# Kernel optimization log

Measured on AMD Instinct MI355X. Metric: run time of the kernel, lower is better.

The kernel has to match this reference:

```python
import jax, jax.numpy as jnp
import numpy as np
from jax import lax

VOCAB = 50257; IN_DIM = 1024; MEM = 1024
ATT_UNITS = 256; HOPS = 16
H1 = 1024; H2 = 512; H3 = 256; CLASSES = 5
N = 512  # maxlen == number of tree nodes (pad() is a no-op, penalty mask is zero)


def _build_tree(n):
    # Binary heap tree relabeled to DFS post-order ranks, so children always
    # have smaller rank than their parent and H accumulates in the same order
    # as the original recursive torch code.
    order = []
    def post(j):
        for c in (2 * j + 1, 2 * j + 2):
            if c < n:
                post(c)
        order.append(j)
    post(0)
    rank = {j: r for r, j in enumerate(order)}
    child_idx = np.zeros((n, 2), np.int32)
    mask = np.zeros((n, 2), np.float32)
    for j in range(n):
        r = rank[j]
        for k, c in enumerate((2 * j + 1, 2 * j + 2)):
            if c < n:
                child_idx[r, k] = rank[c]
                mask[r, k] = 1.0
    return jnp.asarray(child_idx), jnp.asarray(mask)


def setup_inputs() -> dict:
    key = jax.random.key(0)
    ks = jax.random.split(key, 24)
    def w(k, shape, s=0.05):
        return jax.random.normal(k, shape, jnp.float32) * s
    child_idx, child_mask = _build_tree(N)
    return {
        "linputs": jax.random.randint(ks[0], (N,), 0, VOCAB, jnp.int32),
        "rinputs": jax.random.randint(ks[1], (N,), 0, VOCAB, jnp.int32),
        "child_idx": child_idx,
        "child_mask": child_mask,
        "emb": w(ks[2], (VOCAB, IN_DIM)),
        "w_ioux": w(ks[3], (3 * MEM, IN_DIM)), "b_ioux": w(ks[4], (3 * MEM,)),
        "w_iouh": w(ks[5], (3 * MEM, MEM)), "b_iouh": w(ks[6], (3 * MEM,)),
        "w_fx": w(ks[7], (MEM, IN_DIM)), "b_fx": w(ks[8], (MEM,)),
        "w_fh": w(ks[9], (MEM, MEM)), "b_fh": w(ks[10], (MEM,)),
        "ws1": w(ks[11], (ATT_UNITS, MEM)),
        "ws2": w(ks[12], (HOPS, ATT_UNITS)),
        "wf": w(ks[13], (1, MEM, H1)),
        "w_lat": w(ks[14], (1, HOPS)), "b_lat": w(ks[15], (1,)),
        "w_fc": w(ks[16], (H2, 3 * H1)), "b_fc": w(ks[17], (H2,)),
        "w_out": w(ks[18], (H3, H2)), "b_out": w(ks[19], (H3,)),
        "w_out1": w(ks[20], (CLASSES, H3)), "b_out1": w(ks[21], (CLASSES,)),
    }


def _tree_lstm(x, child_idx, child_mask, w_ioux, b_ioux, w_iouh, b_iouh,
               w_fx, b_fx, w_fh, b_fh):
    # x: [N, in_dim]; nodes in post-order (children before parent).
    # Leaf case of the original (single all-zero child) is reproduced exactly
    # by masked (zero) child rows: child_h_sum = 0 and sum(f * child_c) = 0.
    n = x.shape[0]
    mem = w_fh.shape[0]
    x_iou = x @ w_ioux.T + b_ioux  # [N, 3M], precomputed input projections
    x_f = x @ w_fx.T + b_fx        # [N, M]

    def step(carry, xs):
        C, Hs = carry
        i, ci, m, xiou, xf = xs
        ch = Hs[ci] * m[:, None]   # [2, M] masked child hidden states
        cc = C[ci] * m[:, None]    # [2, M] masked child cell states
        iou = xiou + ch.sum(0) @ w_iouh.T + b_iouh
        ig, og, ug = jnp.split(iou, 3)
        ig = jax.nn.sigmoid(ig); og = jax.nn.sigmoid(og); ug = jnp.tanh(ug)
        f = jax.nn.sigmoid(ch @ w_fh.T + b_fh + xf)  # [2, M] forget per child
        c = ig * ug + (f * cc).sum(0)
        h = og * jnp.tanh(c)
        return (C.at[i].set(c), Hs.at[i].set(h)), None

    z = jnp.zeros((n, mem), x.dtype)
    (C, Hs), _ = lax.scan(step, (z, z),
                          (jnp.arange(n), child_idx, child_mask, x_iou, x_f))
    return Hs  # H stacked in DFS post-order; root hidden is Hs[-1]


def _attend(H, ws1, ws2):
    # H: [N, M]; N == maxlen so the penalty term of the original is all-zero.
    hbar = jnp.tanh(H @ ws1.T)                           # [N, att_units]
    alphas = jax.nn.softmax((hbar @ ws2.T).T, axis=-1)   # [hops, N]
    return alphas @ H, alphas[None]                      # [hops, M], [1, hops, N]


def reference(linputs, rinputs, child_idx, child_mask, emb,
              w_ioux, b_ioux, w_iouh, b_iouh, w_fx, b_fx, w_fh, b_fh,
              ws1, ws2, wf, w_lat, b_lat, w_fc, b_fc, w_out, b_out,
              w_out1, b_out1):
    tl = lambda tok: _tree_lstm(emb[tok], child_idx, child_mask,
                                w_ioux, b_ioux, w_iouh, b_iouh,
                                w_fx, b_fx, w_fh, b_fh)
    Hl = tl(linputs)
    Hr = tl(rinputs)
    Ml, attl = _attend(Hl, ws1, ws2)
    Mr, attr = _attend(Hr, ws1, ws2)
    lstate = jax.nn.relu(Ml @ wf[0])   # [hops, H1]
    rstate = jax.nn.relu(Mr @ wf[0])
    # lat_att applied on transposed matrix == left-multiply by its weight row
    lvec = w_lat @ lstate + b_lat      # [1, H1]
    rvec = w_lat @ rstate + b_lat
    fr = jnp.concatenate([jnp.abs(lvec - rvec), lvec * rvec,
                          0.5 * (lvec + rvec)], axis=1)  # [1, 3*H1]
    fc = jax.nn.leaky_relu(fr @ w_fc.T + b_fc, 0.01)
    fc2 = jax.nn.sigmoid(fc @ w_out.T + b_out)
    out = jax.nn.log_softmax(fc2 @ w_out1.T + b_out1, axis=-1)  # [1, classes]
    return out, attl, attr
```

## Files before the change

kernel.cpp:

```cpp
#include <hip/hip_runtime.h>
#include <math.h>

#define NN 512
#define MEMD 1024

typedef __attribute__((ext_vector_type(8))) short short8;
typedef __attribute__((ext_vector_type(4))) float float4v;

struct Sched {
  int child0[NN]; int child1[NN];
  float m0[NN]; float m1[NN];
  int chrow[2 * NN];
  int order[NN];
  int lvl_off[12];
};

constexpr void post_order_rec(int j, int n, int (&ord)[NN], int& cnt) {
  if (2 * j + 1 < n) post_order_rec(2 * j + 1, n, ord, cnt);
  if (2 * j + 2 < n) post_order_rec(2 * j + 2, n, ord, cnt);
  ord[cnt++] = j;
}

constexpr Sched make_sched() {
  Sched s{};
  int ord[NN] = {}; int cnt = 0;
  post_order_rec(0, NN, ord, cnt);
  int rank[NN] = {};
  for (int r = 0; r < NN; ++r) rank[ord[r]] = r;
  for (int j = 0; j < NN; ++j) {
    int r = rank[j];
    int c0 = 2 * j + 1, c1 = 2 * j + 2;
    s.child0[r] = (c0 < NN) ? rank[c0] : 0;
    s.m0[r] = (c0 < NN) ? 1.0f : 0.0f;
    s.child1[r] = (c1 < NN) ? rank[c1] : 0;
    s.m1[r] = (c1 < NN) ? 1.0f : 0.0f;
  }
  int h[NN] = {};
  for (int r = 0; r < NN; ++r) {
    int hh = 0;
    if (s.m0[r] > 0.0f) { int t = h[s.child0[r]] + 1; if (t > hh) hh = t; }
    if (s.m1[r] > 0.0f) { int t = h[s.child1[r]] + 1; if (t > hh) hh = t; }
    h[r] = hh;
  }
  int counts[12] = {};
  for (int r = 0; r < NN; ++r) counts[h[r]]++;
  s.lvl_off[0] = 0;
  for (int l = 0; l < 11; ++l) s.lvl_off[l + 1] = s.lvl_off[l] + counts[l];
  int pos[12] = {};
  for (int l = 0; l < 12; ++l) pos[l] = s.lvl_off[l];
  for (int r = 0; r < NN; ++r) s.order[pos[h[r]]++] = r;
  for (int slot = 0; slot < NN; ++slot) {
    int r = s.order[slot];
    s.chrow[2 * slot + 0] = (s.m0[r] > 0.f) ? s.child0[r] : -1;
    s.chrow[2 * slot + 1] = (s.m1[r] > 0.f) ? s.child1[r] : -1;
  }
  return s;
}

static constexpr Sched g_sched = make_sched();
__constant__ Sched c_sched = g_sched;

__device__ __forceinline__ float sigm(float x) { return 1.0f / (1.0f + expf(-x)); }

__device__ __forceinline__ unsigned short f2bf(float f) {
  union { float f; unsigned int u; } v; v.f = f;
  unsigned int r = v.u + 0x7fffu + ((v.u >> 16) & 1u);
  return (unsigned short)(r >> 16);
}

__device__ __forceinline__ void glds16(const unsigned short* g, unsigned short* l) {
  __builtin_amdgcn_global_load_lds(
      (const __attribute__((address_space(1))) void*)g,
      (__attribute__((address_space(3))) void*)l, 16, 0, 0);
}

__global__ __launch_bounds__(256) void k_cast_w(
    const float* __restrict__ w_ioux, const float* __restrict__ w_fx,
    const float* __restrict__ w_iouh, const float* __restrict__ w_fh,
    unsigned short* __restrict__ Wx, unsigned short* __restrict__ Wh)
{
  const int b = (int)blockIdx.x;
  const float* src; unsigned short* dst;
  if (b < 4096) {
    dst = Wx + (size_t)b * 1024;
    src = (b < 3072) ? w_ioux + (size_t)b * 1024 : w_fx + (size_t)(b - 3072) * 1024;
  } else {
    int r = b - 4096;
    dst = Wh + (size_t)r * 1024;
    src = (r < 3072) ? w_iouh + (size_t)r * 1024 : w_fh + (size_t)(r - 3072) * 1024;
  }
  const int t4 = threadIdx.x * 4;
  float4 v = *(const float4*)(src + t4);
  ushort4 o;
  o.x = f2bf(v.x); o.y = f2bf(v.y); o.z = f2bf(v.z); o.w = f2bf(v.w);
  *(ushort4*)(dst + t4) = o;
}

__global__ __launch_bounds__(256) void k_cast_emb(
    const int* __restrict__ lin, const int* __restrict__ rin,
    const float* __restrict__ emb, unsigned short* __restrict__ Ae)
{
  const int r = (int)blockIdx.x;
  const int tok = (r < 512) ? lin[r] : rin[r - 512];
  const float* src = emb + (size_t)tok * 1024;
  const int t4 = threadIdx.x * 4;
  float4 v = *(const float4*)(src + t4);
  ushort4 o;
  o.x = f2bf(v.x); o.y = f2bf(v.y); o.z = f2bf(v.z); o.w = f2bf(v.w);
  *(ushort4*)(Ae + (size_t)r * 1024 + t4) = o;
}

__global__ void k_zero_row(unsigned short* __restrict__ Hb) {
  unsigned int* p = (unsigned int*)(Hb + (size_t)1024 * 1024);
  p[threadIdx.x] = 0u;
  p[threadIdx.x + 256] = 0u;
}

__global__ __launch_bounds__(256) void k_gemm(
    const unsigned short* __restrict__ A, const unsigned short* __restrict__ B,
    float* __restrict__ Cout, int M, int off, int R)
{
  __shared__ unsigned short As[128 * 64];
  __shared__ unsigned short Bs[128 * 64];
  const int tid = threadIdx.x;
  const int L = tid & 63, w = tid >> 6;
  const int bx = (int)blockIdx.x, by = (int)blockIdx.y;
  const int q = (L & 7) ^ (L >> 3);

  const unsigned short* ga[4];
  const unsigned short* gb[4];
  #pragma unroll
  for (int i = 0; i < 4; ++i) {
    int c = w * 4 + i;
    int r = 8 * c + (L >> 3);
    int u = bx * 128 + r;
    int arow;
    if (off < 0) {
      arow = u;
    } else {
      if (u >= 4 * R) arow = 1024;
      else {
        int t = (u >= 2 * R) ? 1 : 0;
        int rr = u - t * 2 * R;
        int ch = c_sched.chrow[2 * (off + (rr >> 1)) + (rr & 1)];
        arow = (ch < 0) ? 1024 : t * 512 + ch;
      }
    }
    ga[i] = A + (size_t)arow * 1024 + q * 8;
    gb[i] = B + (size_t)(by * 128 + r) * 1024 + q * 8;
  }

  float4v acc[4][4];
  #pragma unroll
  for (int i = 0; i < 4; ++i)
    #pragma unroll
    for (int j = 0; j < 4; ++j) acc[i][j] = (float4v)(0.0f);

  const int wm = (w & 1) * 64, wn = (w >> 1) * 64;
  const int lr = L & 15, lq = L >> 4;

  for (int kk = 0; kk < 16; ++kk) {
    #pragma unroll
    for (int i = 0; i < 4; ++i) {
      glds16(ga[i], As + (w * 4 + i) * 512);
      glds16(gb[i], Bs + (w * 4 + i) * 512);
      ga[i] += 64; gb[i] += 64;
    }
    __syncthreads();
    #pragma unroll
    for (int kh = 0; kh < 2; ++kh) {
      short8 af[4], bf[4];
      #pragma unroll
      for (int mi = 0; mi < 4; ++mi) {
        int tr = wm + mi * 16 + lr;
        af[mi] = *(const short8*)(As + tr * 64 + (((kh * 4 + lq) ^ (tr & 7)) * 8));
      }
      #pragma unroll
      for (int ni = 0; ni < 4; ++ni) {
        int tr = wn + ni * 16 + lr;
        bf[ni] = *(const short8*)(Bs + tr * 64 + (((kh * 4 + lq) ^ (tr & 7)) * 8));
      }
      #pragma unroll
      for (int mi = 0; mi < 4; ++mi)
        #pragma unroll
        for (int ni = 0; ni < 4; ++ni)
          acc[mi][ni] = __builtin_amdgcn_mfma_f32_16x16x32_bf16(
              af[mi], bf[ni], acc[mi][ni], 0, 0, 0);
    }
    __syncthreads();
  }

  #pragma unroll
  for (int mi = 0; mi < 4; ++mi) {
    #pragma unroll
    for (int reg = 0; reg < 4; ++reg) {
      int gr = bx * 128 + wm + mi * 16 + lq * 4 + reg;
      if (gr < M) {
        #pragma unroll
        for (int ni = 0; ni < 4; ++ni) {
          int gc = by * 128 + wn + ni * 16 + lr;
          Cout[(size_t)gr * 4096 + gc] = acc[mi][ni][reg];
        }
      }
    }
  }
}

__global__ __launch_bounds__(256) void k_cell_leaf(
    const float* __restrict__ XO,
    const float* __restrict__ b_ioux, const float* __restrict__ b_iouh,
    float* __restrict__ H, float* __restrict__ C, unsigned short* __restrict__ Hb)
{
  const int s = (int)blockIdx.x;
  const int t = s >> 8, idx = s & 255;
  const int node = c_sched.order[idx];
  const size_t row = (size_t)t * 512 + node;
  for (int d = threadIdx.x; d < MEMD; d += 256) {
    float gi = XO[row * 4096 + d] + b_ioux[d] + b_iouh[d];
    float go = XO[row * 4096 + 1024 + d] + b_ioux[1024 + d] + b_iouh[1024 + d];
    float gu = XO[row * 4096 + 2048 + d] + b_ioux[2048 + d] + b_iouh[2048 + d];
    float cv = sigm(gi) * tanhf(gu);
    float hv = sigm(go) * tanhf(cv);
    C[row * MEMD + d] = cv;
    H[row * MEMD + d] = hv;
    Hb[row * MEMD + d] = f2bf(hv);
  }
}

__global__ __launch_bounds__(256) void k_cell_nl(
    const float* __restrict__ XO, const float* __restrict__ LO,
    const float* __restrict__ b_ioux, const float* __restrict__ b_iouh,
    const float* __restrict__ b_fx, const float* __restrict__ b_fh,
    float* __restrict__ H, float* __restrict__ C, unsigned short* __restrict__ Hb,
    int off, int R)
{
  const int s = (int)blockIdx.x;
  const int t = s / R, idx = s % R;
  const int node = c_sched.order[off + idx];
  const int c0 = c_sched.child0[node], c1 = c_sched.child1[node];
  const float m0 = c_sched.m0[node], m1 = c_sched.m1[node];
  const size_t row = (size_t)t * 512 + node;
  const size_t u0 = (size_t)(2 * s) * 4096;
  const size_t u1 = (size_t)(2 * s + 1) * 4096;
  for (int d = threadIdx.x; d < MEMD; d += 256) {
    float gi = XO[row * 4096 + d] + LO[u0 + d] + LO[u1 + d]
             + b_ioux[d] + b_iouh[d];
    float go = XO[row * 4096 + 1024 + d] + LO[u0 + 1024 + d] + LO[u1 + 1024 + d]
             + b_ioux[1024 + d] + b_iouh[1024 + d];
    float gu = XO[row * 4096 + 2048 + d] + LO[u0 + 2048 + d] + LO[u1 + 2048 + d]
             + b_ioux[2048 + d] + b_iouh[2048 + d];
    float xf = XO[row * 4096 + 3072 + d] + b_fx[d] + b_fh[d];
    float f0 = sigm(LO[u0 + 3072 + d] + xf);
    float f1 = sigm(LO[u1 + 3072 + d] + xf);
    float cc0 = m0 * C[((size_t)t * 512 + c0) * MEMD + d];
    float cc1 = m1 * C[((size_t)t * 512 + c1) * MEMD + d];
    float cv = sigm(gi) * tanhf(gu) + f0 * cc0 + f1 * cc1;
    float hv = sigm(go) * tanhf(cv);
    C[row * MEMD + d] = cv;
    H[row * MEMD + d] = hv;
    Hb[row * MEMD + d] = f2bf(hv);
  }
}

__global__ __launch_bounds__(256) void k_hbar(
    const float* __restrict__ H, const float* __restrict__ ws1,
    float* __restrict__ hbar)
{
  __shared__ float As2[64][17];
  __shared__ float Bs2[64][17];
  const int tid = threadIdx.x;
  const int tx = tid & 15, ty = tid >> 4;
  const int o0 = blockIdx.x * 64;
  const int r0 = blockIdx.y * 64;
  const int e = tid * 4;
  const int lm = e >> 4, lk = e & 15;
  const float* arow = H + (size_t)(r0 + lm) * MEMD;
  const float* brow = ws1 + (size_t)(o0 + lm) * MEMD;

  float acc[4][4] = {};
  for (int k0 = 0; k0 < MEMD; k0 += 16) {
    const float* pa = arow + k0 + lk;
    As2[lm][lk + 0] = pa[0]; As2[lm][lk + 1] = pa[1];
    As2[lm][lk + 2] = pa[2]; As2[lm][lk + 3] = pa[3];
    const float* pb = brow + k0 + lk;
    Bs2[lm][lk + 0] = pb[0]; Bs2[lm][lk + 1] = pb[1];
    Bs2[lm][lk + 2] = pb[2]; Bs2[lm][lk + 3] = pb[3];
    __syncthreads();
    #pragma unroll
    for (int kk = 0; kk < 16; ++kk) {
      float av[4], bv[4];
      #pragma unroll
      for (int i = 0; i < 4; ++i) av[i] = As2[ty * 4 + i][kk];
      #pragma unroll
      for (int j = 0; j < 4; ++j) bv[j] = Bs2[tx * 4 + j][kk];
      #pragma unroll
      for (int i = 0; i < 4; ++i)
        #pragma unroll
        for (int j = 0; j < 4; ++j) acc[i][j] += av[i] * bv[j];
    }
    __syncthreads();
  }
  #pragma unroll
  for (int i = 0; i < 4; ++i) {
    int r = r0 + ty * 4 + i;
    #pragma unroll
    for (int j = 0; j < 4; ++j) {
      int o = o0 + tx * 4 + j;
      hbar[(size_t)r * 256 + o] = tanhf(acc[i][j]);
    }
  }
}

__global__ __launch_bounds__(256) void k_logits(
    const float* __restrict__ hbar, const float* __restrict__ ws2,
    float* __restrict__ logits)
{
  __shared__ float hb[128][65];
  __shared__ float w2[16][256];
  const int b = (int)blockIdx.x;
  const int t = b / 4;
  const int n0 = (b % 4) * 128;
  const int tid = threadIdx.x;
  for (int e2 = tid; e2 < 16 * 256; e2 += 256) w2[e2 / 256][e2 % 256] = ws2[e2];
  const int n = tid & 127;
  const int hbase = (tid >> 7) * 8;
  float acc[8] = {};
  for (int a0 = 0; a0 < 256; a0 += 64) {
    __syncthreads();
    for (int e2 = tid; e2 < 128 * 64; e2 += 256) {
      int rr = e2 >> 6, aa = e2 & 63;
      hb[rr][aa] = hbar[(size_t)(t * 512 + n0 + rr) * 256 + a0 + aa];
    }
    __syncthreads();
    for (int aa = 0; aa < 64; ++aa) {
      float v = hb[n][aa];
      #pragma unroll
      for (int hh = 0; hh < 8; ++hh) acc[hh] += v * w2[hbase + hh][a0 + aa];
    }
  }
  #pragma unroll
  for (int hh = 0; hh < 8; ++hh)
    logits[(size_t)(t * 16 + hbase + hh) * 512 + n0 + n] = acc[hh];
}

__global__ __launch_bounds__(256) void k_softmax(
    const float* __restrict__ logits, float* __restrict__ alphas,
    float* __restrict__ out)
{
  const int b = (int)blockIdx.x;
  const int t = b / 16, h = b % 16;
  const float* lg = logits + (size_t)(t * 16 + h) * 512;
  __shared__ float red[256];
  const int tid = threadIdx.x;
  float v0 = lg[tid], v1 = lg[tid + 256];
  red[tid] = fmaxf(v0, v1);
  __syncthreads();
  for (int s2 = 128; s2 > 0; s2 >>= 1) {
    if (tid < s2) red[tid] = fmaxf(red[tid], red[tid + s2]);
    __syncthreads();
  }
  float mx = red[0];
  __syncthreads();
  float e0 = expf(v0 - mx), e1 = expf(v1 - mx);
  red[tid] = e0 + e1;
  __syncthreads();
  for (int s2 = 128; s2 > 0; s2 >>= 1) {
    if (tid < s2) red[tid] += red[tid + s2];
    __syncthreads();
  }
  float inv = 1.0f / red[0];
  float a0 = e0 * inv, a1 = e1 * inv;
  alphas[(size_t)(t * 16 + h) * 512 + tid] = a0;
  alphas[(size_t)(t * 16 + h) * 512 + tid + 256] = a1;
  out[5 + (size_t)t * 8192 + (size_t)h * 512 + tid] = a0;
  out[5 + (size_t)t * 8192 + (size_t)h * 512 + tid + 256] = a1;
}

__global__ __launch_bounds__(256) void k_attnM(
    const float* __restrict__ alphas, const float* __restrict__ H,
    float* __restrict__ M)
{
  __shared__ float al[16][512];
  const int b = (int)blockIdx.x;
  const int t = b / 4;
  const int m0 = (b % 4) * 256;
  const int tid = threadIdx.x;
  for (int e2 = tid; e2 < 16 * 512; e2 += 256)
    al[e2 >> 9][e2 & 511] = alphas[(size_t)t * 8192 + e2];
  __syncthreads();
  float acc[16] = {};
  for (int n = 0; n < 512; ++n) {
    float hv = H[((size_t)t * 512 + n) * MEMD + m0 + tid];
    #pragma unroll
    for (int h = 0; h < 16; ++h) acc[h] += al[h][n] * hv;
  }
  #pragma unroll
  for (int h = 0; h < 16; ++h)
    M[((size_t)t * 16 + h) * MEMD + m0 + tid] = acc[h];
}

__global__ __launch_bounds__(256) void k_lstate(
    const float* __restrict__ M, const float* __restrict__ wf,
    float* __restrict__ tmp)
{
  __shared__ float Ms[4][1024];
  const int b = (int)blockIdx.x;
  const int t = b / 16;
  const int rem = b % 16;
  const int h0 = (rem / 4) * 4;
  const int o0 = (rem % 4) * 256;
  const int tid = threadIdx.x;
  for (int e2 = tid; e2 < 4 * 1024; e2 += 256)
    Ms[e2 >> 10][e2 & 1023] = M[((size_t)t * 16 + h0 + (e2 >> 10)) * MEMD + (e2 & 1023)];
  __syncthreads();
  float acc[4] = {};
  for (int m = 0; m < 1024; ++m) {
    float wv = wf[(size_t)m * 1024 + o0 + tid];
    #pragma unroll
    for (int h = 0; h < 4; ++h) acc[h] += Ms[h][m] * wv;
  }
  #pragma unroll
  for (int h = 0; h < 4; ++h)
    tmp[((size_t)t * 16 + h0 + h) * 1024 + o0 + tid] = acc[h];
}

__global__ __launch_bounds__(256) void k_fr(
    const float* __restrict__ tmp,
    const float* __restrict__ w_lat, const float* __restrict__ b_lat,
    float* __restrict__ FR)
{
  __shared__ float wl[16];
  const int tid = threadIdx.x;
  if (tid < 16) wl[tid] = w_lat[tid];
  __syncthreads();
  const int o = blockIdx.x * 256 + tid;
  const float blat = b_lat[0];
  float lv = blat, rv = blat;
  #pragma unroll
  for (int h = 0; h < 16; ++h) {
    lv += wl[h] * fmaxf(tmp[(size_t)h * 1024 + o], 0.0f);
    rv += wl[h] * fmaxf(tmp[(size_t)(16 + h) * 1024 + o], 0.0f);
  }
  FR[o] = fabsf(lv - rv);
  FR[1024 + o] = lv * rv;
  FR[2048 + o] = 0.5f * (lv + rv);
}

__global__ __launch_bounds__(256) void k_fc(
    const float* __restrict__ FR, const float* __restrict__ w_fc,
    const float* __restrict__ b_fc, float* __restrict__ FC)
{
  const int j = (int)blockIdx.x;
  const int tid = threadIdx.x;
  const float* wrow = w_fc + (size_t)j * 3072;
  float acc = 0.f;
  #pragma unroll
  for (int i = 0; i < 12; ++i) {
    int k = tid + i * 256;
    acc += FR[k] * wrow[k];
  }
  __shared__ float red[256];
  red[tid] = acc;
  __syncthreads();
  for (int s2 = 128; s2 > 0; s2 >>= 1) {
    if (tid < s2) red[tid] += red[tid + s2];
    __syncthreads();
  }
  if (tid == 0) {
    float v = red[0] + b_fc[j];
    FC[j] = (v > 0.f) ? v : 0.01f * v;
  }
}

__global__ __launch_bounds__(256) void k_fc2(
    const float* __restrict__ FC, const float* __restrict__ w_out,
    const float* __restrict__ b_out, float* __restrict__ FC2)
{
  const int j = (int)blockIdx.x;
  const int tid = threadIdx.x;
  const float* wrow = w_out + (size_t)j * 512;
  float acc = FC[tid] * wrow[tid] + FC[tid + 256] * wrow[tid + 256];
  __shared__ float red[256];
  red[tid] = acc;
  __syncthreads();
  for (int s2 = 128; s2 > 0; s2 >>= 1) {
    if (tid < s2) red[tid] += red[tid + s2];
    __syncthreads();
  }
  if (tid == 0) FC2[j] = 1.0f / (1.0f + expf(-(red[0] + b_out[j])));
}

__global__ __launch_bounds__(320) void k_final(
    const float* __restrict__ FC2,
    const float* __restrict__ w_out1, const float* __restrict__ b_out1,
    float* __restrict__ out)
{
  __shared__ float lg5[5];
  const int tid = threadIdx.x;
  const int cls = tid >> 6;
  const int lane = tid & 63;
  const float* wrow = w_out1 + (size_t)cls * 256;
  float acc = 0.f;
  #pragma unroll
  for (int i = 0; i < 4; ++i) {
    int k = lane + i * 64;
    acc += FC2[k] * wrow[k];
  }
  #pragma unroll
  for (int s2 = 32; s2 > 0; s2 >>= 1) acc += __shfl_down(acc, s2, 64);
  if (lane == 0) lg5[cls] = acc + b_out1[cls];
  __syncthreads();
  if (tid == 0) {
    float mx = lg5[0];
    for (int k = 1; k < 5; ++k) mx = fmaxf(mx, lg5[k]);
    float s2 = 0.f;
    for (int k = 0; k < 5; ++k) s2 += expf(lg5[k] - mx);
    float lse = mx + logf(s2);
    for (int k = 0; k < 5; ++k) out[k] = lg5[k] - lse;
  }
}

extern "C" void kernel_launch(void* const* d_in, const int* in_sizes, int n_in,
                              void* d_out, int out_size, void* d_ws, size_t ws_size,
                              hipStream_t stream)
{
  const int*   lin    = (const int*)d_in[0];
  const int*   rin    = (const int*)d_in[1];
  const float* emb    = (const float*)d_in[4];
  const float* w_ioux = (const float*)d_in[5];
  const float* b_ioux = (const float*)d_in[6];
  const float* w_iouh = (const float*)d_in[7];
  const float* b_iouh = (const float*)d_in[8];
  const float* w_fx   = (const float*)d_in[9];
  const float* b_fx   = (const float*)d_in[10];
  const float* w_fh   = (const float*)d_in[11];
  const float* b_fh   = (const float*)d_in[12];
  const float* ws1    = (const float*)d_in[13];
  const float* ws2    = (const float*)d_in[14];
  const float* wf     = (const float*)d_in[15];
  const float* w_lat  = (const float*)d_in[16];
  const float* b_lat  = (const float*)d_in[17];
  const float* w_fc   = (const float*)d_in[18];
  const float* b_fc   = (const float*)d_in[19];
  const float* w_out  = (const float*)d_in[20];
  const float* b_out  = (const float*)d_in[21];
  const float* w_out1 = (const float*)d_in[22];
  const float* b_out1 = (const float*)d_in[23];
  float* out = (float*)d_out;

  float* fws  = (float*)d_ws;
  float* XO   = fws;
  float* LO   = XO + 1024 * 4096;
  float* H    = LO + 512 * 4096;
  float* C    = H + 1024 * 1024;
  float* HBAR = C + 1024 * 1024;
  float* LG   = HBAR + 1024 * 256;
  float* AL   = LG + 16384;
  float* MB   = AL + 16384;
  float* TMP  = MB + 32768;
  float* FR   = TMP + 32768;
  float* FC   = FR + 3072;
  float* FC2  = FC + 512;
  unsigned short* Ae = (unsigned short*)(FC2 + 256);
  unsigned short* Wx = Ae + 1024 * 1024;
  unsigned short* Wh = Wx = Wx;
  Wx = Ae + 1024 * 1024;
  Wh = Wx + 4096 * 1024;
  unsigned short* Hb = Wh + 4096 * 1024;

  k_cast_w<<<8192, 256, 0, stream>>>(w_ioux, w_fx, w_iouh, w_fh, Wx, Wh);
  k_cast_emb<<<1024, 256, 0, stream>>>(lin, rin, emb, Ae);
  k_zero_row<<<1, 256, 0, stream>>>(Hb);

  k_gemm<<<dim3(8, 32), 256, 0, stream>>>(Ae, Wx, XO, 1024, -1, 0);

  k_cell_leaf<<<512, 256, 0, stream>>>(XO, b_ioux, b_iouh, H, C, Hb);

  for (int l = 1; l < 11; ++l) {
    int off = g_sched.lvl_off[l];
    int R = g_sched.lvl_off[l + 1] - off;
    if (R <= 0) continue;
    int gx = (4 * R + 127) / 128;
    k_gemm<<<dim3(gx, 32), 256, 0, stream>>>(Hb, Wh, LO, 4 * R, off, R);
    k_cell_nl<<<2 * R, 256, 0, stream>>>(XO, LO, b_ioux, b_iouh, b_fx, b_fh,
                                         H, C, Hb, off, R);
  }

  k_hbar<<<dim3(4, 16), 256, 0, stream>>>(H, ws1, HBAR);
  k_logits<<<8, 256, 0, stream>>>(HBAR, ws2, LG);
  k_softmax<<<32, 256, 0, stream>>>(LG, AL, out);
  k_attnM<<<8, 256, 0, stream>>>(AL, H, MB);
  k_lstate<<<32, 256, 0, stream>>>(MB, wf, TMP);
  k_fr<<<4, 256, 0, stream>>>(TMP, w_lat, b_lat, FR);
  k_fc<<<512, 256, 0, stream>>>(FR, w_fc, b_fc, FC);
  k_fc2<<<256, 256, 0, stream>>>(FC, w_out, b_out, FC2);
  k_final<<<1, 320, 0, stream>>>(FC2, w_out1, b_out1, out);
}
```

Before: 779.4 us.

## Fuse entire pipeline into one persistent megakernel with grid barriers

Replaces about 30 separate kernel launches with one persistent 256-block kernel. Stages are separated by atomic grid-wide barriers, which removes per-launch overhead and idle gaps between the many small level-wise tree steps. It also moves the hbar projection onto the bf16 MFMA GEMM path with a transposed tanh output, and reads H from bf16 instead of keeping an fp32 copy. The costs are atomic spin-barrier latency, reduced precision in the attention path, and reliance on all 256 blocks being co-resident.

```diff
diff --git a/kernel.cpp b/kernel.cpp
--- a/kernel.cpp
+++ b/kernel.cpp
@@ -2,7 +2,6 @@
 #include <math.h>
 
 #define NN 512
-#define MEMD 1024
 
 typedef __attribute__((ext_vector_type(8))) short short8;
 typedef __attribute__((ext_vector_type(4))) float float4v;
@@ -68,63 +67,54 @@
   return (unsigned short)(r >> 16);
 }
 
+__device__ __forceinline__ float bf2f(unsigned short b) {
+  union { unsigned int u; float f; } v; v.u = ((unsigned int)b) << 16;
+  return v.f;
+}
+
 __device__ __forceinline__ void glds16(const unsigned short* g, unsigned short* l) {
   __builtin_amdgcn_global_load_lds(
       (const __attribute__((address_space(1))) void*)g,
       (__attribute__((address_space(3))) void*)l, 16, 0, 0);
 }
 
-__global__ __launch_bounds__(256) void k_cast_w(
-    const float* __restrict__ w_ioux, const float* __restrict__ w_fx,
-    const float* __restrict__ w_iouh, const float* __restrict__ w_fh,
-    unsigned short* __restrict__ Wx, unsigned short* __restrict__ Wh)
+__device__ __forceinline__ void gbar(unsigned int* bar) {
+  __syncthreads();
+  if (threadIdx.x == 0) {
+    __hip_atomic_fetch_add(bar, 1u, __ATOMIC_ACQ_REL, __HIP_MEMORY_SCOPE_AGENT);
+    while (__hip_atomic_load(bar, __ATOMIC_ACQUIRE, __HIP_MEMORY_SCOPE_AGENT) < 256u)
+      __builtin_amdgcn_s_sleep(2);
+  }
+  __syncthreads();
+}
+
+struct KParams {
+  const int* lin; const int* rin;
+  const float* emb;
+  const float* w_ioux; const float* b_ioux;
+  const float* w_iouh; const float* b_iouh;
+  const float* w_fx; const float* b_fx;
+  const float* w_fh; const float* b_fh;
+  const float* ws1; const float* ws2;
+  const float* wf; const float* w_lat; const float* b_lat;
+  const float* w_fc; const float* b_fc;
+  const float* w_out; const float* b_out;
+  const float* w_out1; const float* b_out1;
+  float* out;
+  unsigned int* bars;
+  float* XO; float* LO; float* C; float* hbarT;
+  float* AL; float* MB; float* TMP; float* FR; float* FC; float* FC2;
+  unsigned short* Ae; unsigned short* Wx; unsigned short* Wh;
+  unsigned short* ws1b; unsigned short* Hb;
+};
+
+__device__ void gemm_tile(const KParams& p,
+    const unsigned short* __restrict__ A, const unsigned short* __restrict__ B,
+    float* __restrict__ Cout, unsigned short* As, unsigned short* Bs,
+    int bx, int by, int M, int off, int R, int mode)
 {
-  const int b = (int)blockIdx.x;
-  const float* src; unsigned short* dst;
-  if (b < 4096) {
-    dst = Wx + (size_t)b * 1024;
-    src = (b < 3072) ? w_ioux + (size_t)b * 1024 : w_fx + (size_t)(b - 3072) * 1024;
-  } else {
-    int r = b - 4096;
-    dst = Wh + (size_t)r * 1024;
-    src = (r < 3072) ? w_iouh + (size_t)r * 1024 : w_fh + (size_t)(r - 3072) * 1024;
-  }
-  const int t4 = threadIdx.x * 4;
-  float4 v = *(const float4*)(src + t4);
-  ushort4 o;
-  o.x = f2bf(v.x); o.y = f2bf(v.y); o.z = f2bf(v.z); o.w = f2bf(v.w);
-  *(ushort4*)(dst + t4) = o;
-}
-
-__global__ __launch_bounds__(256) void k_cast_emb(
-    const int* __restrict__ lin, const int* __restrict__ rin,
-    const float* __restrict__ emb, unsigned short* __restrict__ Ae)
-{
-  const int r = (int)blockIdx.x;
-  const int tok = (r < 512) ? lin[r] : rin[r - 512];
-  const float* src = emb + (size_t)tok * 1024;
-  const int t4 = threadIdx.x * 4;
-  float4 v = *(const float4*)(src + t4);
-  ushort4 o;
-  o.x = f2bf(v.x); o.y = f2bf(v.y); o.z = f2bf(v.z); o.w = f2bf(v.w);
-  *(ushort4*)(Ae + (size_t)r * 1024 + t4) = o;
-}
-
-__global__ void k_zero_row(unsigned short* __restrict__ Hb) {
-  unsigned int* p = (unsigned int*)(Hb + (size_t)1024 * 1024);
-  p[threadIdx.x] = 0u;
-  p[threadIdx.x + 256] = 0u;
-}
-
-__global__ __launch_bounds__(256) void k_gemm(
-    const unsigned short* __restrict__ A, const unsigned short* __restrict__ B,
-    float* __restrict__ Cout, int M, int off, int R)
-{
-  __shared__ unsigned short As[128 * 64];
-  __shared__ unsigned short Bs[128 * 64];
   const int tid = threadIdx.x;
   const int L = tid & 63, w = tid >> 6;
-  const int bx = (int)blockIdx.x, by = (int)blockIdx.y;
   const int q = (L & 7) ^ (L >> 3);
 
   const unsigned short* ga[4];
@@ -135,9 +125,7 @@
     int r = 8 * c + (L >> 3);
     int u = bx * 128 + r;
     int arow;
-    if (off < 0) {
-      arow = u;
-    } else {
+    if (mode == 1) {
       if (u >= 4 * R) arow = 1024;
       else {
         int t = (u >= 2 * R) ? 1 : 0;
@@ -145,6 +133,8 @@
         int ch = c_sched.chrow[2 * (off + (rr >> 1)) + (rr & 1)];
         arow = (ch < 0) ? 1024 : t * 512 + ch;
       }
+    } else {
+      arow = u;
     }
     ga[i] = A + (size_t)arow * 1024 + q * 8;
     gb[i] = B + (size_t)(by * 128 + r) * 1024 + q * 8;
@@ -190,51 +180,51 @@
     __syncthreads();
   }
 
-  #pragma unroll
-  for (int mi = 0; mi < 4; ++mi) {
-    #pragma unroll
-    for (int reg = 0; reg < 4; ++reg) {
-      int gr = bx * 128 + wm + mi * 16 + lq * 4 + reg;
-      if (gr < M) {
+  if (mode == 2) {
+    #pragma unroll
+    for (int mi = 0; mi < 4; ++mi)
+      #pragma unroll
+      for (int reg = 0; reg < 4; ++reg) {
+        int gr = bx * 128 + wm + mi * 16 + lq * 4 + reg;
         #pragma unroll
         for (int ni = 0; ni < 4; ++ni) {
           int gc = by * 128 + wn + ni * 16 + lr;
-          Cout[(size_t)gr * 4096 + gc] = acc[mi][ni][reg];
+          p.hbarT[(size_t)gc * 1024 + gr] = tanhf(acc[mi][ni][reg]);
         }
       }
-    }
-  }
-}
-
-__global__ __launch_bounds__(256) void k_cell_leaf(
-    const float* __restrict__ XO,
-    const float* __restrict__ b_ioux, const float* __restrict__ b_iouh,
-    float* __restrict__ H, float* __restrict__ C, unsigned short* __restrict__ Hb)
-{
-  const int s = (int)blockIdx.x;
+  } else {
+    #pragma unroll
+    for (int mi = 0; mi < 4; ++mi)
+      #pragma unroll
+      for (int reg = 0; reg < 4; ++reg) {
+        int gr = bx * 128 + wm + mi * 16 + lq * 4 + reg;
+        if (gr < M) {
+          #pragma unroll
+          for (int ni = 0; ni < 4; ++ni) {
+            int gc = by * 128 + wn + ni * 16 + lr;
+            Cout[(size_t)gr * 4096 + gc] = acc[mi][ni][reg];
+          }
+        }
+      }
+  }
+}
+
+__device__ void cell_leaf(const KParams& p, int s) {
   const int t = s >> 8, idx = s & 255;
   const int node = c_sched.order[idx];
   const size_t row = (size_t)t * 512 + node;
-  for (int d = threadIdx.x; d < MEMD; d += 256) {
-    float gi = XO[row * 4096 + d] + b_ioux[d] + b_iouh[d];
-    float go = XO[row * 4096 + 1024 + d] + b_ioux[1024 + d] + b_iouh[1024 + d];
-    float gu = XO[row * 4096 + 2048 + d] + b_ioux[2048 + d] + b_iouh[2048 + d];
+  for (int d = threadIdx.x; d < 1024; d += 256) {
+    float gi = p.XO[row * 4096 + d] + p.b_ioux[d] + p.b_iouh[d];
+    float go = p.XO[row * 4096 + 1024 + d] + p.b_ioux[1024 + d] + p.b_iouh[1024 + d];
+    float gu = p.XO[row * 4096 + 2048 + d] + p.b_ioux[2048 + d] + p.b_iouh[2048 + d];
     float cv = sigm(gi) * tanhf(gu);
     float hv = sigm(go) * tanhf(cv);
-    C[row * MEMD + d] = cv;
-    H[row * MEMD + d] = hv;
-    Hb[row * MEMD + d] = f2bf(hv);
-  }
-}
-
-__global__ __launch_bounds__(256) void k_cell_nl(
-    const float* __restrict__ XO, const float* __restrict__ LO,
-    const float* __restrict__ b_ioux, const float* __restrict__ b_iouh,
-    const float* __restrict__ b_fx, const float* __restrict__ b_fh,
-    float* __restrict__ H, float* __restrict__ C, unsigned short* __restrict__ Hb,
-    int off, int R)
-{
-  const int s = (int)blockIdx.x;
+    p.C[row * 1024 + d] = cv;
+    p.Hb[row * 1024 + d] = f2bf(hv);
+  }
+}
+
+__device__ void cell_nl(const KParams& p, int s, int off, int R) {
   const int t = s / R, idx = s % R;
   const int node = c_sched.order[off + idx];
   const int c0 = c_sched.child0[node], c1 = c_sched.child1[node];
@@ -242,281 +232,246 @@
   const size_t row = (size_t)t * 512 + node;
   const size_t u0 = (size_t)(2 * s) * 4096;
   const size_t u1 = (size_t)(2 * s + 1) * 4096;
-  for (int d = threadIdx.x; d < MEMD; d += 256) {
-    float gi = XO[row * 4096 + d] + LO[u0 + d] + LO[u1 + d]
-             + b_ioux[d] + b_iouh[d];
-    float go = XO[row * 4096 + 1024 + d] + LO[u0 + 1024 + d] + LO[u1 + 1024 + d]
-             + b_ioux[1024 + d] + b_iouh[1024 + d];
-    float gu = XO[row * 4096 + 2048 + d] + LO[u0 + 2048 + d] + LO[u1 + 2048 + d]
-             + b_ioux[2048 + d] + b_iouh[2048 + d];
-    float xf = XO[row * 4096 + 3072 + d] + b_fx[d] + b_fh[d];
-    float f0 = sigm(LO[u0 + 3072 + d] + xf);
-    float f1 = sigm(LO[u1 + 3072 + d] + xf);
-    float cc0 = m0 * C[((size_t)t * 512 + c0) * MEMD + d];
-    float cc1 = m1 * C[((size_t)t * 512 + c1) * MEMD + d];
+  for (int d = threadIdx.x; d < 1024; d += 256) {
+    float gi = p.XO[row * 4096 + d] + p.LO[u0 + d] + p.LO[u1 + d]
+             + p.b_ioux[d] + p.b_iouh[d];
+    float go = p.XO[row * 4096 + 1024 + d] + p.LO[u0 + 1024 + d] + p.LO[u1 + 1024 + d]
+             + p.b_ioux[1024 + d] + p.b_iouh[1024 + d];
+    float gu = p.XO[row * 4096 + 2048 + d] + p.LO[u0 + 2048 + d] + p.LO[u1 + 2048 + d]
+             + p.b_ioux[2048 + d] + p.b_iouh[2048 + d];
+    float xf = p.XO[row * 4096 + 3072 + d] + p.b_fx[d] + p.b_fh[d];
+    float f0 = sigm(p.LO[u0 + 3072 + d] + xf);
+    float f1 = sigm(p.LO[u1 + 3072 + d] + xf);
+    float cc0 = m0 * p.C[((size_t)t * 512 + c0) * 1024 + d];
+    float cc1 = m1 * p.C[((size_t)t * 512 + c1) * 1024 + d];
     float cv = sigm(gi) * tanhf(gu) + f0 * cc0 + f1 * cc1;
     float hv = sigm(go) * tanhf(cv);
-    C[row * MEMD + d] = cv;
-    H[row * MEMD + d] = hv;
-    Hb[row * MEMD + d] = f2bf(hv);
-  }
-}
-
-__global__ __launch_bounds__(256) void k_hbar(
-    const float* __restrict__ H, const float* __restrict__ ws1,
-    float* __restrict__ hbar)
+    p.C[row * 1024 + d] = cv;
+    p.Hb[row * 1024 + d] = f2bf(hv);
+  }
+}
+
+__global__ __launch_bounds__(256, 1) void mega(KParams p)
 {
-  __shared__ float As2[64][17];
-  __shared__ float Bs2[64][17];
+  __shared__ __align__(16) unsigned char SMEM[36864];
+  unsigned short* As = (unsigned short*)SMEM;
+  unsigned short* Bs = (unsigned short*)(SMEM + 16384);
+  const int bid = (int)blockIdx.x;
   const int tid = threadIdx.x;
-  const int tx = tid & 15, ty = tid >> 4;
-  const int o0 = blockIdx.x * 64;
-  const int r0 = blockIdx.y * 64;
-  const int e = tid * 4;
-  const int lm = e >> 4, lk = e & 15;
-  const float* arow = H + (size_t)(r0 + lm) * MEMD;
-  const float* brow = ws1 + (size_t)(o0 + lm) * MEMD;
-
-  float acc[4][4] = {};
-  for (int k0 = 0; k0 < MEMD; k0 += 16) {
-    const float* pa = arow + k0 + lk;
-    As2[lm][lk + 0] = pa[0]; As2[lm][lk + 1] = pa[1];
-    As2[lm][lk + 2] = pa[2]; As2[lm][lk + 3] = pa[3];
-    const float* pb = brow + k0 + lk;
-    Bs2[lm][lk + 0] = pb[0]; Bs2[lm][lk + 1] = pb[1];
-    Bs2[lm][lk + 2] = pb[2]; Bs2[lm][lk + 3] = pb[3];
-    __syncthreads();
-    #pragma unroll
-    for (int kk = 0; kk < 16; ++kk) {
-      float av[4], bv[4];
-      #pragma unroll
-      for (int i = 0; i < 4; ++i) av[i] = As2[ty * 4 + i][kk];
-      #pragma unroll
-      for (int j = 0; j < 4; ++j) bv[j] = Bs2[tx * 4 + j][kk];
-      #pragma unroll
-      for (int i = 0; i < 4; ++i)
-        #pragma unroll
-        for (int j = 0; j < 4; ++j) acc[i][j] += av[i] * bv[j];
-    }
-    __syncthreads();
-  }
-  #pragma unroll
-  for (int i = 0; i < 4; ++i) {
-    int r = r0 + ty * 4 + i;
-    #pragma unroll
-    for (int j = 0; j < 4; ++j) {
-      int o = o0 + tx * 4 + j;
-      hbar[(size_t)r * 256 + o] = tanhf(acc[i][j]);
-    }
-  }
-}
-
-__global__ __launch_bounds__(256) void k_logits(
-    const float* __restrict__ hbar, const float* __restrict__ ws2,
-    float* __restrict__ logits)
-{
-  __shared__ float hb[128][65];
-  __shared__ float w2[16][256];
-  const int b = (int)blockIdx.x;
-  const int t = b / 4;
-  const int n0 = (b % 4) * 128;
-  const int tid = threadIdx.x;
-  for (int e2 = tid; e2 < 16 * 256; e2 += 256) w2[e2 / 256][e2 % 256] = ws2[e2];
-  const int n = tid & 127;
-  const int hbase = (tid >> 7) * 8;
-  float acc[8] = {};
-  for (int a0 = 0; a0 < 256; a0 += 64) {
-    __syncthreads();
-    for (int e2 = tid; e2 < 128 * 64; e2 += 256) {
-      int rr = e2 >> 6, aa = e2 & 63;
-      hb[rr][aa] = hbar[(size_t)(t * 512 + n0 + rr) * 256 + a0 + aa];
-    }
-    __syncthreads();
-    for (int aa = 0; aa < 64; ++aa) {
-      float v = hb[n][aa];
-      #pragma unroll
-      for (int hh = 0; hh < 8; ++hh) acc[hh] += v * w2[hbase + hh][a0 + aa];
-    }
-  }
-  #pragma unroll
-  for (int hh = 0; hh < 8; ++hh)
-    logits[(size_t)(t * 16 + hbase + hh) * 512 + n0 + n] = acc[hh];
-}
-
-__global__ __launch_bounds__(256) void k_softmax(
-    const float* __restrict__ logits, float* __restrict__ alphas,
-    float* __restrict__ out)
-{
-  const int b = (int)blockIdx.x;
-  const int t = b / 16, h = b % 16;
-  const float* lg = logits + (size_t)(t * 16 + h) * 512;
-  __shared__ float red[256];
-  const int tid = threadIdx.x;
-  float v0 = lg[tid], v1 = lg[tid + 256];
-  red[tid] = fmaxf(v0, v1);
-  __syncthreads();
-  for (int s2 = 128; s2 > 0; s2 >>= 1) {
-    if (tid < s2) red[tid] = fmaxf(red[tid], red[tid + s2]);
-    __syncthreads();
-  }
-  float mx = red[0];
-  __syncthreads();
-  float e0 = expf(v0 - mx), e1 = expf(v1 - mx);
-  red[tid] = e0 + e1;
-  __syncthreads();
-  for (int s2 = 128; s2 > 0; s2 >>= 1) {
-    if (tid < s2) red[tid] += red[tid + s2];
-    __syncthreads();
-  }
-  float inv = 1.0f / red[0];
-  float a0 = e0 * inv, a1 = e1 * inv;
-  alphas[(size_t)(t * 16 + h) * 512 + tid] = a0;
-  alphas[(size_t)(t * 16 + h) * 512 + tid + 256] = a1;
-  out[5 + (size_t)t * 8192 + (size_t)h * 512 + tid] = a0;
-  out[5 + (size_t)t * 8192 + (size_t)h * 512 + tid + 256] = a1;
-}
-
-__global__ __launch_bounds__(256) void k_attnM(
-    const float* __restrict__ alphas, const float* __restrict__ H,
-    float* __restrict__ M)
-{
-  __shared__ float al[16][512];
-  const int b = (int)blockIdx.x;
-  const int t = b / 4;
-  const int m0 = (b % 4) * 256;
-  const int tid = threadIdx.x;
-  for (int e2 = tid; e2 < 16 * 512; e2 += 256)
-    al[e2 >> 9][e2 & 511] = alphas[(size_t)t * 8192 + e2];
-  __syncthreads();
-  float acc[16] = {};
-  for (int n = 0; n < 512; ++n) {
-    float hv = H[((size_t)t * 512 + n) * MEMD + m0 + tid];
-    #pragma unroll
-    for (int h = 0; h < 16; ++h) acc[h] += al[h][n] * hv;
-  }
-  #pragma unroll
-  for (int h = 0; h < 16; ++h)
-    M[((size_t)t * 16 + h) * MEMD + m0 + tid] = acc[h];
-}
-
-__global__ __launch_bounds__(256) void k_lstate(
-    const float* __restrict__ M, const float* __restrict__ wf,
-    float* __restrict__ tmp)
-{
-  __shared__ float Ms[4][1024];
-  const int b = (int)blockIdx.x;
-  const int t = b / 16;
-  const int rem = b % 16;
-  const int h0 = (rem / 4) * 4;
-  const int o0 = (rem % 4) * 256;
-  const int tid = threadIdx.x;
-  for (int e2 = tid; e2 < 4 * 1024; e2 += 256)
-    Ms[e2 >> 10][e2 & 1023] = M[((size_t)t * 16 + h0 + (e2 >> 10)) * MEMD + (e2 & 1023)];
-  __syncthreads();
-  float acc[4] = {};
-  for (int m = 0; m < 1024; ++m) {
-    float wv = wf[(size_t)m * 1024 + o0 + tid];
-    #pragma unroll
-    for (int h = 0; h < 4; ++h) acc[h] += Ms[h][m] * wv;
-  }
-  #pragma unroll
-  for (int h = 0; h < 4; ++h)
-    tmp[((size_t)t * 16 + h0 + h) * 1024 + o0 + tid] = acc[h];
-}
-
-__global__ __launch_bounds__(256) void k_fr(
-    const float* __restrict__ tmp,
-    const float* __restrict__ w_lat, const float* __restrict__ b_lat,
-    float* __restrict__ FR)
-{
-  __shared__ float wl[16];
-  const int tid = threadIdx.x;
-  if (tid < 16) wl[tid] = w_lat[tid];
-  __syncthreads();
-  const int o = blockIdx.x * 256 + tid;
-  const float blat = b_lat[0];
-  float lv = blat, rv = blat;
-  #pragma unroll
-  for (int h = 0; h < 16; ++h) {
-    lv += wl[h] * fmaxf(tmp[(size_t)h * 1024 + o], 0.0f);
-    rv += wl[h] * fmaxf(tmp[(size_t)(16 + h) * 1024 + o], 0.0f);
-  }
-  FR[o] = fabsf(lv - rv);
-  FR[1024 + o] = lv * rv;
-  FR[2048 + o] = 0.5f * (lv + rv);
-}
-
-__global__ __launch_bounds__(256) void k_fc(
-    const float* __restrict__ FR, const float* __restrict__ w_fc,
-    const float* __restrict__ b_fc, float* __restrict__ FC)
-{
-  const int j = (int)blockIdx.x;
-  const int tid = threadIdx.x;
-  const float* wrow = w_fc + (size_t)j * 3072;
-  float acc = 0.f;
-  #pragma unroll
-  for (int i = 0; i < 12; ++i) {
-    int k = tid + i * 256;
-    acc += FR[k] * wrow[k];
-  }
-  __shared__ float red[256];
-  red[tid] = acc;
-  __syncthreads();
-  for (int s2 = 128; s2 > 0; s2 >>= 1) {
-    if (tid < s2) red[tid] += red[tid + s2];
-    __syncthreads();
-  }
-  if (tid == 0) {
-    float v = red[0] + b_fc[j];
-    FC[j] = (v > 0.f) ? v : 0.01f * v;
-  }
-}
-
-__global__ __launch_bounds__(256) void k_fc2(
-    const float* __restrict__ FC, const float* __restrict__ w_out,
-    const float* __restrict__ b_out, float* __restrict__ FC2)
-{
-  const int j = (int)blockIdx.x;
-  const int tid = threadIdx.x;
-  const float* wrow = w_out + (size_t)j * 512;
-  float acc = FC[tid] * wrow[tid] + FC[tid + 256] * wrow[tid + 256];
-  __shared__ float red[256];
-  red[tid] = acc;
-  __syncthreads();
-  for (int s2 = 128; s2 > 0; s2 >>= 1) {
-    if (tid < s2) red[tid] += red[tid + s2];
-    __syncthreads();
-  }
-  if (tid == 0) FC2[j] = 1.0f / (1.0f + expf(-(red[0] + b_out[j])));
-}
-
-__global__ __launch_bounds__(320) void k_final(
-    const float* __restrict__ FC2,
-    const float* __restrict__ w_out1, const float* __restrict__ b_out1,
-    float* __restrict__ out)
-{
-  __shared__ float lg5[5];
-  const int tid = threadIdx.x;
-  const int cls = tid >> 6;
-  const int lane = tid & 63;
-  const float* wrow = w_out1 + (size_t)cls * 256;
-  float acc = 0.f;
-  #pragma unroll
-  for (int i = 0; i < 4; ++i) {
-    int k = lane + i * 64;
-    acc += FC2[k] * wrow[k];
-  }
-  #pragma unroll
-  for (int s2 = 32; s2 > 0; s2 >>= 1) acc += __shfl_down(acc, s2, 64);
-  if (lane == 0) lg5[cls] = acc + b_out1[cls];
-  __syncthreads();
-  if (tid == 0) {
-    float mx = lg5[0];
-    for (int k = 1; k < 5; ++k) mx = fmaxf(mx, lg5[k]);
-    float s2 = 0.f;
-    for (int k = 0; k < 5; ++k) s2 += expf(lg5[k] - mx);
-    float lse = mx + logf(s2);
-    for (int k = 0; k < 5; ++k) out[k] = lg5[k] - lse;
+  const int G = 256;
+  int bix = 0;
+
+  for (int task = bid; task <= 9472; task += G) {
+    if (task == 9472) {
+      *(ushort4*)(p.Hb + (size_t)1024 * 1024 + tid * 4) = ushort4{0, 0, 0, 0};
+      continue;
+    }
+    const float* src; unsigned short* dst;
+    if (task < 4096) {
+      dst = p.Wx + (size_t)task * 1024;
+      src = (task < 3072) ? p.w_ioux + (size_t)task * 1024
+                          : p.w_fx + (size_t)(task - 3072) * 1024;
+    } else if (task < 8192) {
+      int r = task - 4096;
+      dst = p.Wh + (size_t)r * 1024;
+      src = (r < 3072) ? p.w_iouh + (size_t)r * 1024
+                       : p.w_fh + (size_t)(r - 3072) * 1024;
+    } else if (task < 9216) {
+      int r = task - 8192;
+      int tok = (r < 512) ? p.lin[r] : p.rin[r - 512];
+      dst = p.Ae + (size_t)r * 1024;
+      src = p.emb + (size_t)tok * 1024;
+    } else {
+      int r = task - 9216;
+      dst = p.ws1b + (size_t)r * 1024;
+      src = p.ws1 + (size_t)r * 1024;
+    }
+    const int t4 = tid * 4;
+    float4 v = *(const float4*)(src + t4);
+    ushort4 o;
+    o.x = f2bf(v.x); o.y = f2bf(v.y); o.z = f2bf(v.z); o.w = f2bf(v.w);
+    *(ushort4*)(dst + t4) = o;
+  }
+  gbar(&p.bars[bix++]);
+
+  for (int task = bid; task < 256; task += G)
+    gemm_tile(p, p.Ae, p.Wx, p.XO, As, Bs, task >> 5, task & 31, 1024, 0, 0, 0);
+  gbar(&p.bars[bix++]);
+
+  for (int s = bid; s < 512; s += G) cell_leaf(p, s);
+  gbar(&p.bars[bix++]);
+
+  for (int l = 1; l <= 10; ++l) {
+    const int off = c_sched.lvl_off[l];
+    const int R = c_sched.lvl_off[l + 1] - off;
+    if (R <= 0) continue;
+    const int gx = (4 * R + 127) / 128;
+    const int ntile = gx * 32;
+    for (int task = bid; task < ntile; task += G)
+      gemm_tile(p, p.Hb, p.Wh, p.LO, As, Bs, task >> 5, task & 31, 4 * R, off, R, 1);
+    gbar(&p.bars[bix++]);
+    for (int s = bid; s < 2 * R; s += G) cell_nl(p, s, off, R);
+    gbar(&p.bars[bix++]);
+  }
+
+  for (int task = bid; task < 16; task += G)
+    gemm_tile(p, p.Hb, p.ws1b, nullptr, As, Bs, task >> 1, task & 1, 1024, 0, 0, 2);
+  gbar(&p.bars[bix++]);
+
+  for (int task = bid; task < 32; task += G) {
+    const int t = task >> 4, h = task & 15;
+    float* w2row = (float*)SMEM;
+    float* red = (float*)(SMEM + 2048);
+    w2row[tid] = p.ws2[h * 256 + tid];
+    __syncthreads();
+    float a0 = 0.f, a1 = 0.f;
+    #pragma unroll 4
+    for (int a = 0; a < 256; ++a) {
+      float wv = w2row[a];
+      const float* hrow = p.hbarT + (size_t)a * 1024 + t * 512;
+      a0 += wv * hrow[tid];
+      a1 += wv * hrow[tid + 256];
+    }
+    red[tid] = fmaxf(a0, a1);
+    __syncthreads();
+    for (int s2 = 128; s2 > 0; s2 >>= 1) {
+      if (tid < s2) red[tid] = fmaxf(red[tid], red[tid + s2]);
+      __syncthreads();
+    }
+    float mx = red[0];
+    __syncthreads();
+    float e0 = expf(a0 - mx), e1 = expf(a1 - mx);
+    red[tid] = e0 + e1;
+    __syncthreads();
+    for (int s2 = 128; s2 > 0; s2 >>= 1) {
+      if (tid < s2) red[tid] += red[tid + s2];
+      __syncthreads();
+    }
+    float inv = 1.0f / red[0];
+    float v0 = e0 * inv, v1 = e1 * inv;
+    p.AL[(size_t)(t * 16 + h) * 512 + tid] = v0;
+    p.AL[(size_t)(t * 16 + h) * 512 + tid + 256] = v1;
+    p.out[5 + (size_t)t * 8192 + (size_t)h * 512 + tid] = v0;
+    p.out[5 + (size_t)t * 8192 + (size_t)h * 512 + tid + 256] = v1;
+  }
+  gbar(&p.bars[bix++]);
+
+  for (int task = bid; task < 8; task += G) {
+    const int t = task >> 2;
+    const int m0 = (task & 3) * 256;
+    float* al = (float*)SMEM;
+    for (int e = tid; e < 8192; e += 256) al[e] = p.AL[(size_t)t * 8192 + e];
+    __syncthreads();
+    float acc[16] = {};
+    for (int n = 0; n < 512; ++n) {
+      float hv = bf2f(p.Hb[((size_t)t * 512 + n) * 1024 + m0 + tid]);
+      #pragma unroll
+      for (int h = 0; h < 16; ++h) acc[h] += al[h * 512 + n] * hv;
+    }
+    #pragma unroll
+    for (int h = 0; h < 16; ++h)
+      p.MB[((size_t)t * 16 + h) * 1024 + m0 + tid] = acc[h];
+  }
+  gbar(&p.bars[bix++]);
+
+  for (int task = bid; task < 32; task += G) {
+    const int t = task / 16;
+    const int rem = task % 16;
+    const int h0 = (rem / 4) * 4;
+    const int o0 = (rem % 4) * 256;
+    float* Ms = (float*)SMEM;
+    for (int e = tid; e < 4096; e += 256)
+      Ms[e] = p.MB[((size_t)t * 16 + h0 + (e >> 10)) * 1024 + (e & 1023)];
+    __syncthreads();
+    float acc[4] = {};
+    for (int m = 0; m < 1024; ++m) {
+      float wv = p.wf[(size_t)m * 1024 + o0 + tid];
+      #pragma unroll
+      for (int h = 0; h < 4; ++h) acc[h] += Ms[h * 1024 + m] * wv;
+    }
+    #pragma unroll
+    for (int h = 0; h < 4; ++h)
+      p.TMP[((size_t)t * 16 + h0 + h) * 1024 + o0 + tid] = acc[h];
+  }
+  gbar(&p.bars[bix++]);
+
+  for (int task = bid; task < 4; task += G) {
+    float* wl = (float*)SMEM;
+    if (tid < 16) wl[tid] = p.w_lat[tid];
+    __syncthreads();
+    const int o = task * 256 + tid;
+    const float blat = p.b_lat[0];
+    float lv = blat, rv = blat;
+    #pragma unroll
+    for (int h = 0; h < 16; ++h) {
+      lv += wl[h] * fmaxf(p.TMP[(size_t)h * 1024 + o], 0.0f);
+      rv += wl[h] * fmaxf(p.TMP[(size_t)(16 + h) * 1024 + o], 0.0f);
+    }
+    p.FR[o] = fabsf(lv - rv);
+    p.FR[1024 + o] = lv * rv;
+    p.FR[2048 + o] = 0.5f * (lv + rv);
+  }
+  gbar(&p.bars[bix++]);
+
+  {
+    float* red = (float*)SMEM;
+    for (int j = bid; j < 512; j += G) {
+      const float* wrow = p.w_fc + (size_t)j * 3072;
+      float acc = 0.f;
+      #pragma unroll
+      for (int i = 0; i < 12; ++i) {
+        int k = tid + i * 256;
+        acc += p.FR[k] * wrow[k];
+      }
+      red[tid] = acc;
+      __syncthreads();
+      for (int s2 = 128; s2 > 0; s2 >>= 1) {
+        if (tid < s2) red[tid] += red[tid + s2];
+        __syncthreads();
+      }
+      if (tid == 0) {
+        float v = red[0] + p.b_fc[j];
+        p.FC[j] = (v > 0.f) ? v : 0.01f * v;
+      }
+      __syncthreads();
+    }
+  }
+  gbar(&p.bars[bix++]);
+
+  {
+    float* red = (float*)SMEM;
+    for (int j = bid; j < 256; j += G) {
+      const float* wrow = p.w_out + (size_t)j * 512;
+      float acc = p.FC[tid] * wrow[tid] + p.FC[tid + 256] * wrow[tid + 256];
+      red[tid] = acc;
+      __syncthreads();
+      for (int s2 = 128; s2 > 0; s2 >>= 1) {
+        if (tid < s2) red[tid] += red[tid + s2];
+        __syncthreads();
+      }
+      if (tid == 0) p.FC2[j] = 1.0f / (1.0f + expf(-(red[0] + p.b_out[j])));
+      __syncthreads();
+    }
+  }
+  gbar(&p.bars[bix++]);
+
+  if (bid == 0) {
+    float* lg5 = (float*)SMEM;
+    if (tid < 5) {
+      float acc = p.b_out1[tid];
+      const float* wrow = p.w_out1 + (size_t)tid * 256;
+      for (int k = 0; k < 256; ++k) acc += p.FC2[k] * wrow[k];
+      lg5[tid] = acc;
+    }
+    __syncthreads();
+    if (tid == 0) {
+      float mx = lg5[0];
+      for (int k = 1; k < 5; ++k) mx = fmaxf(mx, lg5[k]);
+      float s2 = 0.f;
+      for (int k = 0; k < 5; ++k) s2 += expf(lg5[k] - mx);
+      float lse = mx + logf(s2);
+      for (int k = 0; k < 5; ++k) p.out[k] = lg5[k] - lse;
+    }
   }
 }
 
@@ -524,75 +479,49 @@
                               void* d_out, int out_size, void* d_ws, size_t ws_size,
                               hipStream_t stream)
 {
-  const int*   lin    = (const int*)d_in[0];
-  const int*   rin    = (const int*)d_in[1];
-  const float* emb    = (const float*)d_in[4];
-  const float* w_ioux = (const float*)d_in[5];
-  const float* b_ioux = (const float*)d_in[6];
-  const float* w_iouh = (const float*)d_in[7];
-  const float* b_iouh = (const float*)d_in[8];
-  const float* w_fx   = (const float*)d_in[9];
-  const float* b_fx   = (const float*)d_in[10];
-  const float* w_fh   = (const float*)d_in[11];
-  const float* b_fh   = (const float*)d_in[12];
-  const float* ws1    = (const float*)d_in[13];
-  const float* ws2    = (const float*)d_in[14];
-  const float* wf     = (const float*)d_in[15];
-  const float* w_lat  = (const float*)d_in[16];
-  const float* b_lat  = (const float*)d_in[17];
-  const float* w_fc   = (const float*)d_in[18];
-  const float* b_fc   = (const float*)d_in[19];
-  const float* w_out  = (const float*)d_in[20];
-  const float* b_out  = (const float*)d_in[21];
-  const float* w_out1 = (const float*)d_in[22];
-  const float* b_out1 = (const float*)d_in[23];
-  float* out = (float*)d_out;
-
-  float* fws  = (float*)d_ws;
-  float* XO   = fws;
-  float* LO   = XO + 1024 * 4096;
-  float* H    = LO + 512 * 4096;
-  float* C    = H + 1024 * 1024;
-  float* HBAR = C + 1024 * 1024;
-  float* LG   = HBAR + 1024 * 256;
-  float* AL   = LG + 16384;
-  float* MB   = AL + 16384;
-  float* TMP  = MB + 32768;
-  float* FR   = TMP + 32768;
-  float* FC   = FR + 3072;
-  float* FC2  = FC + 512;
-  unsigned short* Ae = (unsigned short*)(FC2 + 256);
-  unsigned short* Wx = Ae + 1024 * 1024;
-  unsigned short* Wh = Wx = Wx;
-  Wx = Ae + 1024 * 1024;
-  Wh = Wx + 4096 * 1024;
-  unsigned short* Hb = Wh + 4096 * 1024;
-
-  k_cast_w<<<8192, 256, 0, stream>>>(w_ioux, w_fx, w_iouh, w_fh, Wx, Wh);
-  k_cast_emb<<<1024, 256, 0, stream>>>(lin, rin, emb, Ae);
-  k_zero_row<<<1, 256, 0, stream>>>(Hb);
-
-  k_gemm<<<dim3(8, 32), 256, 0, stream>>>(Ae, Wx, XO, 1024, -1, 0);
-
-  k_cell_leaf<<<512, 256, 0, stream>>>(XO, b_ioux, b_iouh, H, C, Hb);
-
-  for (int l = 1; l < 11; ++l) {
-    int off = g_sched.lvl_off[l];
-    int R = g_sched.lvl_off[l + 1] - off;
-    if (R <= 0) continue;
-    int gx = (4 * R + 127) / 128;
-    k_gemm<<<dim3(gx, 32), 256, 0, stream>>>(Hb, Wh, LO, 4 * R, off, R);
-    k_cell_nl<<<2 * R, 256, 0, stream>>>(XO, LO, b_ioux, b_iouh, b_fx, b_fh,
-                                         H, C, Hb, off, R);
-  }
-
-  k_hbar<<<dim3(4, 16), 256, 0, stream>>>(H, ws1, HBAR);
-  k_logits<<<8, 256, 0, stream>>>(HBAR, ws2, LG);
-  k_softmax<<<32, 256, 0, stream>>>(LG, AL, out);
-  k_attnM<<<8, 256, 0, stream>>>(AL, H, MB);
-  k_lstate<<<32, 256, 0, stream>>>(MB, wf, TMP);
-  k_fr<<<4, 256, 0, stream>>>(TMP, w_lat, b_lat, FR);
-  k_fc<<<512, 256, 0, stream>>>(FR, w_fc, b_fc, FC);
-  k_fc2<<<256, 256, 0, stream>>>(FC, w_out, b_out, FC2);
-  k_final<<<1, 320, 0, stream>>>(FC2, w_out1, b_out1, out);
-}
+  KParams p;
+  p.lin    = (const int*)d_in[0];
+  p.rin    = (const int*)d_in[1];
+  p.emb    = (const float*)d_in[4];
+  p.w_ioux = (const float*)d_in[5];
+  p.b_ioux = (const float*)d_in[6];
+  p.w_iouh = (const float*)d_in[7];
+  p.b_iouh = (const float*)d_in[8];
+  p.w_fx   = (const float*)d_in[9];
+  p.b_fx   = (const float*)d_in[10];
+  p.w_fh   = (const float*)d_in[11];
+  p.b_fh   = (const float*)d_in[12];
+  p.ws1    = (const float*)d_in[13];
+  p.ws2    = (const float*)d_in[14];
+  p.wf     = (const float*)d_in[15];
+  p.w_lat  = (const float*)d_in[16];
+  p.b_lat  = (const float*)d_in[17];
+  p.w_fc   = (const float*)d_in[18];
+  p.b_fc   = (const float*)d_in[19];
+  p.w_out  = (const float*)d_in[20];
+  p.b_out  = (const float*)d_in[21];
+  p.w_out1 = (const float*)d_in[22];
+  p.b_out1 = (const float*)d_in[23];
+  p.out    = (float*)d_out;
+
+  p.bars = (unsigned int*)d_ws;
+  float* fws = (float*)((char*)d_ws + 256);
+  p.XO    = fws;
+  p.LO    = p.XO + 1024 * 4096;
+  p.C     = p.LO + 512 * 4096;
+  p.hbarT = p.C + 1024 * 1024;
+  p.AL    = p.hbarT + 256 * 1024;
+  p.MB    = p.AL + 16384;
+  p.TMP   = p.MB + 32768;
+  p.FR    = p.TMP + 32768;
+  p.FC    = p.FR + 3072;
+  p.FC2   = p.FC + 512;
+  p.Ae    = (unsigned short*)(p.FC2 + 256);
+  p.Wx    = p.Ae + 1024 * 1024;
+  p.Wh    = p.Wx + 4096 * 1024;
+  p.ws1b  = p.Wh + 4096 * 1024;
+  p.Hb    = p.ws1b + 256 * 1024;
+
+  hipMemsetAsync(d_ws, 0, 256, stream);
+  mega<<<dim3(256), dim3(256), 0, stream>>>(p);
+}
```

New measurement: 1.775 ms. 128% more time.
